# Optimization experiments

Measured on AMD Instinct MI355X. Metric: run time of the kernel, lower is better.

## Reference

```python
import jax, jax.numpy as jnp
import numpy as np
import math

NHEADS = 8


def pos_encoding_2d(d_model, H, W):
    dm = d_model // 2
    div = jnp.exp(jnp.arange(0, dm, 2, dtype=jnp.float32) * (-math.log(10000.0) / dm))  # [dm//2]
    pw = jnp.arange(W, dtype=jnp.float32)[:, None] * div  # [W, dm//2]
    ph = jnp.arange(H, dtype=jnp.float32)[:, None] * div  # [H, dm//2]
    pe = jnp.zeros((d_model, H, W), jnp.float32)
    pe = pe.at[0:dm:2].set(jnp.broadcast_to(jnp.sin(pw).T[:, None, :], (dm // 2, H, W)))
    pe = pe.at[1:dm:2].set(jnp.broadcast_to(jnp.cos(pw).T[:, None, :], (dm // 2, H, W)))
    pe = pe.at[dm::2].set(jnp.broadcast_to(jnp.sin(ph).T[:, :, None], (dm // 2, H, W)))
    pe = pe.at[dm + 1::2].set(jnp.broadcast_to(jnp.cos(ph).T[:, :, None], (dm // 2, H, W)))
    return pe


def conv_same(x, w, b):
    y = jax.lax.conv_general_dilated(x, w, (1, 1), 'SAME',
                                     dimension_numbers=('NCHW', 'OIHW', 'NCHW'))
    return y + b[None, :, None, None]


def layernorm(x, g, b, eps=1e-5):
    mu = x.mean(-1, keepdims=True)
    var = ((x - mu) ** 2).mean(-1, keepdims=True)
    return (x - mu) / jnp.sqrt(var + eps) * g + b


def setup_inputs() -> dict:
    key = jax.random.key(0)
    B, C, H, W = 8, 256, 32, 32
    KQV, NH, K = 64, NHEADS, 3
    ks = jax.random.split(key, 16)
    s_conv = 1.0 / math.sqrt(C * K * K)
    s_lin = 1.0 / math.sqrt(NH * KQV)
    s_ff = 1.0 / math.sqrt(C)
    return {
        'x': jax.random.normal(ks[0], (B, C, H, W), jnp.float32),
        'Wk': jax.random.normal(ks[1], (NH * KQV, C, K, K), jnp.float32) * s_conv,
        'bk': jax.random.normal(ks[2], (NH * KQV,), jnp.float32) * s_conv,
        'Wq': jax.random.normal(ks[3], (NH * KQV, C, K, K), jnp.float32) * s_conv,
        'bq': jax.random.normal(ks[4], (NH * KQV,), jnp.float32) * s_conv,
        'Wv': jax.random.normal(ks[5], (NH * KQV, C, K, K), jnp.float32) * s_conv,
        'bv': jax.random.normal(ks[6], (NH * KQV,), jnp.float32) * s_conv,
        'Wproj': jax.random.normal(ks[7], (C, NH * KQV), jnp.float32) * s_lin,
        'bproj': jax.random.normal(ks[8], (C,), jnp.float32) * s_lin,
        'ln_g': jnp.ones((C,), jnp.float32),
        'ln_b': jnp.zeros((C,), jnp.float32),
        'W1': jax.random.normal(ks[9], (C, C), jnp.float32) * s_ff,
        'b1': jax.random.normal(ks[10], (C,), jnp.float32) * s_ff,
        'W2': jax.random.normal(ks[11], (C, C), jnp.float32) * s_ff,
        'b2': jax.random.normal(ks[12], (C,), jnp.float32) * s_ff,
    }


def reference(x, Wk, bk, Wq, bq, Wv, bv, Wproj, bproj, ln_g, ln_b, W1, b1, W2, b2):
    B, C, H, W = x.shape
    N = H * W
    pe = pos_encoding_2d(C, H, W)
    xp = x + pe[None]                                   # [B,C,H,W]
    xflat = xp.reshape(B, C, N).transpose(0, 2, 1)      # [B,N,C]

    def heads(w, b):
        return conv_same(xp, w, b).reshape(B, NHEADS, -1, N)  # [B,h,c,N]

    k = heads(Wk, bk)
    q = heads(Wq, bq)
    v = heads(Wv, bv)
    scores = jnp.einsum('bhcn,bhcm->bhnm', k, q) / N    # K^T Q / N, [B,h,N,N]
    sm = jax.nn.softmax(scores, axis=1)                 # Softmax2d -> over HEAD dim (faithful)
    att = jnp.einsum('bhnm,bhcm->bhnc', sm, v)          # [B,h,N,c]
    att = att.transpose(0, 2, 3, 1).reshape(B, N, -1)   # [B,N,c*h] (channel-major, head-minor)
    attproj = att @ Wproj.T + bproj                     # [B,N,C]
    addnormed = layernorm(xflat + attproj, ln_g, ln_b)
    h1 = addnormed @ W1.T + b1
    h1 = jnp.where(h1 > 0, h1, 0.1 * h1)                # LeakyReLU(0.1)
    h2 = h1 @ W2.T + b2
    out = layernorm(h2 + addnormed, ln_g, ln_b)         # same LN params reused (faithful)
    return out.transpose(0, 2, 1).reshape(B, C, H, W)
```

## Files before the change

kernel.cpp:

```cpp
#include <hip/hip_runtime.h>
#include <stdint.h>

typedef __attribute__((ext_vector_type(8))) short short8;
typedef __attribute__((ext_vector_type(4))) short s16x4;
typedef __attribute__((ext_vector_type(4))) float f32x4;

#define DEVI __device__ __forceinline__

#if __has_builtin(__builtin_amdgcn_mfma_f32_16x16x16_bf16)
#define MFMA16(a, b, c) __builtin_amdgcn_mfma_f32_16x16x16_bf16(a, b, c, 0, 0, 0)
#else
#define MFMA16(a, b, c) __builtin_amdgcn_mfma_f32_16x16x16bf16_1k(a, b, c, 0, 0, 0)
#endif

DEVI unsigned short f2bf(float f) {
  union { float f; uint32_t u; } v; v.f = f;
  return (unsigned short)((v.u + 0x7fffu + ((v.u >> 16) & 1u)) >> 16);
}

DEVI float bf2f(uint32_t hi16) {
  union { uint32_t u; float f; } v; v.u = hi16;
  return v.f;
}

DEVI uint32_t pkbf(float a, float b) {
  union { float f; uint32_t u; } x, y; x.f = a; y.f = b;
  return ((x.u + 0x8000u) >> 16) | (((y.u + 0x8000u) >> 16) << 16);
}

DEVI void gload_lds16(const void* g, void* l) {
  __builtin_amdgcn_global_load_lds(
      (const __attribute__((address_space(1))) uint32_t*)g,
      (__attribute__((address_space(3))) uint32_t*)l, 16, 0, 0);
}

__global__ void k_petab(float* __restrict__ T, float* __restrict__ zp) {
  int c = threadIdx.x;
  zp[c] = 0.0f;
  int idx = ((c >= 128) ? c - 128 : c) >> 1;
  float freq = expf(-(float)idx * (logf(10000.0f) / 64.0f));
  for (int p = 0; p < 32; ++p) {
    float ang = (float)p * freq;
    T[c * 32 + p] = (c & 1) ? cosf(ang) : sinf(ang);
  }
}

__global__ __launch_bounds__(256) void k_xpt(const float* __restrict__ x,
                                             const float* __restrict__ T,
                                             unsigned short* __restrict__ xpt_bf,
                                             float* __restrict__ xpt_f) {
  __shared__ __align__(16) float tile[32][36];
  const int b = blockIdx.z, c0 = blockIdx.x * 32, n0 = blockIdx.y * 32;
  const int t = threadIdx.x;
  {
    const int cl = t >> 3, ng = (t & 7) * 4;
    const int c = c0 + cl;
    float4 v = *(const float4*)(x + ((size_t)b * 256 + c) * 1024 + n0 + ng);
    float p0, p1, p2, p3;
    if (c < 128) {
      p0 = T[c * 32 + ng + 0]; p1 = T[c * 32 + ng + 1];
      p2 = T[c * 32 + ng + 2]; p3 = T[c * 32 + ng + 3];
    } else {
      p0 = p1 = p2 = p3 = T[c * 32 + (n0 >> 5)];
    }
    tile[ng + 0][cl] = v.x + p0;
    tile[ng + 1][cl] = v.y + p1;
    tile[ng + 2][cl] = v.z + p2;
    tile[ng + 3][cl] = v.w + p3;
  }
  __syncthreads();
  {
    const int nl = t >> 3, cg = (t & 7) * 4;
    float o0 = tile[nl][cg + 0], o1 = tile[nl][cg + 1];
    float o2 = tile[nl][cg + 2], o3 = tile[nl][cg + 3];
    size_t row = (size_t)b * 1024 + n0 + nl;
    *(float4*)(xpt_f + row * 256 + c0 + cg) = make_float4(o0, o1, o2, o3);
    uint32_t lo = (uint32_t)f2bf(o0) | ((uint32_t)f2bf(o1) << 16);
    uint32_t hi = (uint32_t)f2bf(o2) | ((uint32_t)f2bf(o3) << 16);
    *(uint2*)(xpt_bf + row * 256 + c0 + cg) = make_uint2(lo, hi);
  }
}

__global__ void k_packall(const float* __restrict__ Wk, const float* __restrict__ Wq,
                          const float* __restrict__ Wv, const float* __restrict__ bk,
                          const float* __restrict__ bq, const float* __restrict__ bv,
                          const float* __restrict__ Wproj, const float* __restrict__ W1,
                          const float* __restrict__ W2, unsigned short* __restrict__ Wpack,
                          float* __restrict__ bias_kqv, unsigned short* __restrict__ WprojP,
                          unsigned short* __restrict__ W1b, unsigned short* __restrict__ W2b) {
  int bid = blockIdx.x;
  if (bid < 13824) {
    int i = bid * 256 + threadIdx.x;
    if (i >= 1536 * 2304) return;
    int o = i / 2304, kn = i % 2304;
    int ci = kn & 255, khw = kn >> 8;
    const float* src = (o < 512) ? Wk : ((o < 1024) ? Wq : Wv);
    int oo = o & 511;
    Wpack[i] = f2bf(src[((size_t)oo * 256 + ci) * 9 + khw]);
  } else {
    int i = (bid - 13824) * 256 + threadIdx.x;
    if (i < 1536)
      bias_kqv[i] = (i < 512) ? bk[i] : ((i < 1024) ? bq[i - 512] : bv[i - 1024]);
    {
      int j = i >> 9, f = i & 511;
      int h = f >> 6, c = f & 63;
      unsigned short v = f2bf(Wproj[(size_t)j * 512 + c * 8 + h]);
      WprojP[(size_t)j * 1024 + f] = v;
      WprojP[(size_t)j * 1024 + 512 + f] = v;
    }
    if (i < 65536) {
      W1b[i] = f2bf(W1[i]);
      W2b[i] = f2bf(W2[i]);
    }
  }
}

__global__ __launch_bounds__(256, 2) void k_gemm_conv(const unsigned short* __restrict__ xpt,
                                                      const unsigned short* __restrict__ Wp,
                                                      unsigned short* __restrict__ kqv,
                                                      const float* __restrict__ bias,
                                                      const char* __restrict__ zp) {
  __shared__ __align__(16) unsigned short As[2][128 * 64];
  __shared__ __align__(16) unsigned short Bs[2][192 * 64];
  const int tid = threadIdx.x, l = tid & 63, w = tid >> 6;
  const int wm = w >> 1, wn = w & 1, g = l >> 4, ln = l & 15;
  const int m0 = blockIdx.x * 128, n0 = blockIdx.y * 192;
  const int swz = (l & 7) ^ (l >> 3);

  const char* pAbase[4];
#pragma unroll
  for (int j = 0; j < 4; ++j) {
    int r = m0 + (w * 4 + j) * 8 + (l >> 3);
    pAbase[j] = (const char*)xpt + ((size_t)r * 256 + swz * 8) * 2;
  }
  const char* pB0 = (const char*)Wp +
                    ((size_t)(n0 + w * 48 + (l >> 3)) * 2304 + swz * 8) * 2;

  f32x4 acc[4][6] = {};
  int vmask = 0;
  int aoff = 0;

  auto setTap = [&](int tap) {
    int d3 = (tap * 11) >> 5;
    int dy = d3 - 1, dx = tap - d3 * 3 - 1;
    aoff = (dy * 32 + dx) * 512;
    int m = 0;
#pragma unroll
    for (int j = 0; j < 4; ++j) {
      int r = m0 + (w * 4 + j) * 8 + (l >> 3);
      int y = ((r >> 5) & 31) + dy;
      int x = (r & 31) + dx;
      if (((unsigned)y < 32u) && ((unsigned)x < 32u)) m |= (1 << j);
    }
    vmask = m;
  };

  auto STAGE = [&](int buf, int kb) {
#pragma unroll
    for (int j = 0; j < 4; ++j) {
      const char* a = (vmask & (1 << j)) ? (pAbase[j] + aoff) : zp;
      gload_lds16(a, (char*)As + buf * 16384 + (w * 4 + j) * 1024);
    }
#pragma unroll
    for (int j = 0; j < 6; ++j) {
      gload_lds16(pB0 + j * 36864 + kb, (char*)Bs + buf * 24576 + (w * 6 + j) * 1024);
    }
  };

  auto COMPUTE = [&](int buf) {
    const char* Ab2 = (const char*)As + buf * 16384;
    const char* Bb2 = (const char*)Bs + buf * 24576;
#pragma unroll
    for (int kk = 0; kk < 2; ++kk) {
      short8 af[4], bfr[6];
#pragma unroll
      for (int fm = 0; fm < 4; ++fm)
        af[fm] = *(const short8*)(Ab2 + (wm * 64 + fm * 16 + ln) * 128 +
                                  (((kk * 4 + g) ^ (ln & 7)) * 16));
#pragma unroll
      for (int fn = 0; fn < 6; ++fn)
        bfr[fn] = *(const short8*)(Bb2 + (wn * 96 + fn * 16 + ln) * 128 +
                                   (((kk * 4 + g) ^ (ln & 7)) * 16));
#pragma unroll
      for (int fm = 0; fm < 4; ++fm)
#pragma unroll
        for (int fn = 0; fn < 6; ++fn)
          acc[fm][fn] = __builtin_amdgcn_mfma_f32_16x16x32_bf16(af[fm], bfr[fn], acc[fm][fn], 0, 0, 0);
    }
  };

  setTap(0);
  STAGE(0, 0);
  aoff += 128;
  int kb = 128;
  for (int s = 0; s < 36; ++s) {
    const int buf = s & 1;
    if (s < 35) {
      if (((s + 1) & 3) == 0) setTap((s + 1) >> 2);
      STAGE(buf ^ 1, kb);
      kb += 128;
      aoff += 128;
      asm volatile("s_waitcnt vmcnt(10)" ::: "memory");
    } else {
      asm volatile("s_waitcnt vmcnt(0)" ::: "memory");
    }
    __builtin_amdgcn_s_barrier();
    __builtin_amdgcn_sched_barrier(0);
    COMPUTE(buf);
    asm volatile("s_waitcnt lgkmcnt(0)" ::: "memory");
    __builtin_amdgcn_s_barrier();
    __builtin_amdgcn_sched_barrier(0);
  }

#pragma unroll
  for (int fm = 0; fm < 4; ++fm)
#pragma unroll
    for (int fn = 0; fn < 6; ++fn) {
      int col = n0 + wn * 96 + fn * 16 + ln;
      float bb = bias[col];
#pragma unroll
      for (int r = 0; r < 4; ++r) {
        int row = m0 + wm * 64 + fm * 16 + g * 4 + r;
        kqv[(size_t)row * 1536 + col] = f2bf(acc[fm][fn][r] + bb);
      }
    }
}

__global__ __launch_bounds__(256) void k_ffn1(const unsigned short* __restrict__ A,
                                              const unsigned short* __restrict__ B,
                                              unsigned short* __restrict__ Cout,
                                              const float* __restrict__ bias) {
  __shared__ __align__(16) unsigned short As[128 * 64];
  __shared__ __align__(16) unsigned short Bs[64 * 64];
  const int tid = threadIdx.x, l = tid & 63, w = tid >> 6;
  const int g = l >> 4, ln = l & 15;
  const int m0 = blockIdx.x * 128, n0 = blockIdx.y * 64;
  const int swz = (l & 7) ^ (l >> 3);
  f32x4 acc[2][4] = {};

  for (int kt = 0; kt < 256; kt += 64) {
#pragma unroll
    for (int j = 0; j < 4; ++j) {
      int seg = w * 4 + j;
      int r8 = seg * 8 + (l >> 3);
      gload_lds16((const char*)A + ((size_t)(m0 + r8) * 256 + kt + swz * 8) * 2,
                  (char*)As + seg * 1024);
    }
#pragma unroll
    for (int j = 0; j < 2; ++j) {
      int seg = w * 2 + j;
      int r8 = seg * 8 + (l >> 3);
      gload_lds16((const char*)B + ((size_t)(n0 + r8) * 256 + kt + swz * 8) * 2,
                  (char*)Bs + seg * 1024);
    }
    __syncthreads();
#pragma unroll
    for (int kk = 0; kk < 2; ++kk) {
      short8 af[2], bfr[4];
#pragma unroll
      for (int fm = 0; fm < 2; ++fm)
        af[fm] = *(const short8*)((const char*)As + (w * 32 + fm * 16 + ln) * 128 +
                                  (((kk * 4 + g) ^ (ln & 7)) * 16));
#pragma unroll
      for (int fn = 0; fn < 4; ++fn)
        bfr[fn] = *(const short8*)((const char*)Bs + (fn * 16 + ln) * 128 +
                                   (((kk * 4 + g) ^ (ln & 7)) * 16));
#pragma unroll
      for (int fm = 0; fm < 2; ++fm)
#pragma unroll
        for (int fn = 0; fn < 4; ++fn)
          acc[fm][fn] = __builtin_amdgcn_mfma_f32_16x16x32_bf16(af[fm], bfr[fn], acc[fm][fn], 0, 0, 0);
    }
    __syncthreads();
  }

#pragma unroll
  for (int fm = 0; fm < 2; ++fm)
#pragma unroll
    for (int fn = 0; fn < 4; ++fn)
#pragma unroll
      for (int r = 0; r < 4; ++r) {
        int row = m0 + w * 32 + fm * 16 + g * 4 + r;
        int col = n0 + fn * 16 + ln;
        float v = acc[fm][fn][r] + bias[col];
        v = (v > 0.f) ? v : 0.1f * v;
        Cout[(size_t)row * 256 + col] = f2bf(v);
      }
}

__global__ __launch_bounds__(512, 4) void k_attn(const unsigned short* __restrict__ kqv,
                                                 unsigned short* __restrict__ part) {
  __shared__ __align__(16) unsigned short Qs[16][512];
  __shared__ __align__(16) unsigned short Vlin[16][512];
  __shared__ __align__(16) unsigned short Vs[32][16][16];
  __shared__ __align__(16) float sums[4][2][64][4];
  const int tid = threadIdx.x, l = tid & 63, w = tid >> 6;
  const int g = l >> 4, ln = l & 15;
  const int nt = w & 1, hg = w >> 1;
  const int id = blockIdx.x;
  const int b = id & 7, ng = (id >> 3) & 31, ch = id >> 8;
  const int n0 = ng * 32 + nt * 16;
  const int m_base = ch * 512;
  const size_t rowBase = (size_t)b * 1024;
  const float SC = 1.0f / 1024.0f;

  short8 ak[2][2];
#pragma unroll
  for (int hl = 0; hl < 2; ++hl)
#pragma unroll
    for (int kk = 0; kk < 2; ++kk)
      ak[hl][kk] = *(const short8*)&kqv[(rowBase + n0 + ln) * 1536 +
                                        (hg * 2 + hl) * 64 + kk * 32 + g * 8];

  f32x4 acc[2][4] = {};

  const int r0 = w * 2, r1 = w * 2 + 1;
  const char* pRow = (const char*)kqv +
                     (size_t)(rowBase + m_base + r0) * 3072 + 1024 + (size_t)l * 16;
  uint4 q0, q1, v0, v1;

  auto LOADREGS = [&]() {
    q0 = *(const uint4*)pRow;
    v0 = *(const uint4*)(pRow + 1024);
    q1 = *(const uint4*)(pRow + 3072);
    v1 = *(const uint4*)(pRow + 4096);
    pRow += 49152;
  };
  char* const dQ0 = (char*)Qs + r0 * 1024 + ((l ^ (r0 & 7)) * 16);
  char* const dV0 = (char*)Vlin + r0 * 1024 + ((l ^ (r0 & 7)) * 16);
  char* const dQ1 = (char*)Qs + r1 * 1024 + ((l ^ (r1 & 7)) * 16);
  char* const dV1 = (char*)Vlin + r1 * 1024 + ((l ^ (r1 & 7)) * 16);
  auto DSW = [&]() {
    *(uint4*)dQ0 = q0;
    *(uint4*)dV0 = v0;
    *(uint4*)dQ1 = q1;
    *(uint4*)dV1 = v1;
  };

  LOADREGS();
  asm volatile("s_waitcnt vmcnt(0)" ::: "memory");
  DSW();
  asm volatile("s_waitcnt lgkmcnt(0)" ::: "memory");
  __builtin_amdgcn_s_barrier();
  __builtin_amdgcn_sched_barrier(0);

  const uint32_t vsBase = (uint32_t)(uintptr_t)&Vs[0][0][0] + l * 8;

  for (int s = 0; s < 32; ++s) {
    if (s < 31) LOADREGS();

    {
      const int tm = l & 15;
#pragma unroll
      for (int i = 0; i < 2; ++i) {
        int tch = (l >> 4) + w * 4 + i * 32;
        short8 tv = *(const short8*)((const char*)Vlin + tm * 1024 +
                                     ((tch ^ (tm & 7)) * 16));
        *(short8*)((char*)Vs + (tch >> 1) * 512 + tm * 32 + (tch & 1) * 16) = tv;
      }
    }

    f32x4 sv[2] = {};
#pragma unroll
    for (int kk = 0; kk < 2; ++kk)
#pragma unroll
      for (int hl = 0; hl < 2; ++hl) {
        int chq = (hg * 2 + hl) * 8 + kk * 4 + g;
        short8 qa = *(const short8*)((const char*)Qs + ln * 1024 +
                                     ((chq ^ (ln & 7)) * 16));
        sv[hl] = __builtin_amdgcn_mfma_f32_16x16x32_bf16(qa, ak[hl][kk], sv[hl], 0, 0, 0);
      }

    f32x4 e0, e1, ps;
#pragma unroll
    for (int j = 0; j < 4; ++j) {
      e0[j] = __expf(sv[0][j] * SC);
      e1[j] = __expf(sv[1][j] * SC);
      ps[j] = e0[j] + e1[j];
    }
    *(f32x4*)&sums[hg][nt][l][0] = ps;
    asm volatile("s_waitcnt lgkmcnt(0)" ::: "memory");
    __builtin_amdgcn_s_barrier();
    __builtin_amdgcn_sched_barrier(0);

    f32x4 tot = ps;
#pragma unroll
    for (int d = 1; d < 4; ++d) {
      f32x4 o = *(const f32x4*)&sums[(hg + d) & 3][nt][l][0];
      tot[0] += o[0]; tot[1] += o[1]; tot[2] += o[2]; tot[3] += o[3];
    }
    f32x4 inv;
#pragma unroll
    for (int j = 0; j < 4; ++j) inv[j] = __builtin_amdgcn_rcpf(tot[j]);

    s16x4 vf[8];
#pragma unroll
    for (int hl = 0; hl < 2; ++hl) {
      uint32_t ah = vsBase + (hg * 2 + hl) * 2048;
      asm volatile("ds_read_b64_tr_b16 %0, %1" : "=v"(vf[hl * 4 + 0]) : "v"(ah));
      asm volatile("ds_read_b64_tr_b16 %0, %1 offset:512" : "=v"(vf[hl * 4 + 1]) : "v"(ah));
      asm volatile("ds_read_b64_tr_b16 %0, %1 offset:1024" : "=v"(vf[hl * 4 + 2]) : "v"(ah));
      asm volatile("ds_read_b64_tr_b16 %0, %1 offset:1536" : "=v"(vf[hl * 4 + 3]) : "v"(ah));
    }
    asm volatile("s_waitcnt lgkmcnt(0)" ::: "memory");
    __builtin_amdgcn_sched_barrier(0);
    union { uint32_t u[2]; s16x4 v4; } pc0, pc1;
    pc0.u[0] = pkbf(e0[0] * inv[0], e0[1] * inv[1]);
    pc0.u[1] = pkbf(e0[2] * inv[2], e0[3] * inv[3]);
    pc1.u[0] = pkbf(e1[0] * inv[0], e1[1] * inv[1]);
    pc1.u[1] = pkbf(e1[2] * inv[2], e1[3] * inv[3]);
#pragma unroll
    for (int cf = 0; cf < 4; ++cf) {
      acc[0][cf] = MFMA16(vf[cf], pc0.v4, acc[0][cf]);
      acc[1][cf] = MFMA16(vf[4 + cf], pc1.v4, acc[1][cf]);
    }

    if (s < 31) {
      asm volatile("s_waitcnt vmcnt(0)" ::: "memory");
      DSW();
    }
    asm volatile("s_waitcnt lgkmcnt(0)" ::: "memory");
    __builtin_amdgcn_s_barrier();
    __builtin_amdgcn_sched_barrier(0);
  }

  const size_t outBase = (size_t)ch * 8192 * 512 + (rowBase + n0 + ln) * 512;
#pragma unroll
  for (int hl = 0; hl < 2; ++hl)
#pragma unroll
    for (int cf = 0; cf < 4; ++cf)
#pragma unroll
      for (int r2 = 0; r2 < 2; ++r2) {
        int c = (hg * 2 + hl) * 64 + cf * 16 + g * 4 + r2 * 2;
        uint32_t u = (uint32_t)f2bf(acc[hl][cf][2 * r2]) |
                     ((uint32_t)f2bf(acc[hl][cf][2 * r2 + 1]) << 16);
        *(uint32_t*)&part[outBase + c] = u;
      }
}

__global__ __launch_bounds__(256) void k_projln(const unsigned short* __restrict__ part,
                                                const unsigned short* __restrict__ Wp,
                                                const float* __restrict__ bias,
                                                const float* __restrict__ resid,
                                                const float* __restrict__ lg,
                                                const float* __restrict__ lb,
                                                float* __restrict__ out_f,
                                                unsigned short* __restrict__ out_b) {
  __shared__ __align__(16) unsigned short As[32 * 64];
  __shared__ __align__(16) unsigned short Bs[256 * 64];
  __shared__ float rsum[4][32][2];
  const int tid = threadIdx.x, l = tid & 63, w = tid >> 6;
  const int g4 = l >> 4, ln = l & 15;
  const int m0 = blockIdx.x * 32;
  const int swz = (l & 7) ^ (l >> 3);
  f32x4 acc[2][4] = {};

  for (int kt = 0; kt < 1024; kt += 64) {
    gload_lds16((const char*)part + (((size_t)(kt >> 9) * 8192 * 512) +
                                     (size_t)(m0 + w * 8 + (l >> 3)) * 512 +
                                     (kt & 511) + swz * 8) * 2,
                (char*)As + w * 1024);
#pragma unroll
    for (int j = 0; j < 8; ++j) {
      int seg = w * 8 + j;
      gload_lds16((const char*)Wp + ((size_t)(seg * 8 + (l >> 3)) * 1024 + kt + swz * 8) * 2,
                  (char*)Bs + seg * 1024);
    }
    __syncthreads();
#pragma unroll
    for (int kk = 0; kk < 2; ++kk) {
      short8 af[2], bfr[4];
#pragma unroll
      for (int fm = 0; fm < 2; ++fm)
        af[fm] = *(const short8*)((const char*)As + (fm * 16 + ln) * 128 +
                                  (((kk * 4 + g4) ^ (ln & 7)) * 16));
#pragma unroll
      for (int fn = 0; fn < 4; ++fn)
        bfr[fn] = *(const short8*)((const char*)Bs + (w * 64 + fn * 16 + ln) * 128 +
                                   (((kk * 4 + g4) ^ (ln & 7)) * 16));
#pragma unroll
      for (int fm = 0; fm < 2; ++fm)
#pragma unroll
        for (int fn = 0; fn < 4; ++fn)
          acc[fm][fn] = __builtin_amdgcn_mfma_f32_16x16x32_bf16(af[fm], bfr[fn], acc[fm][fn], 0, 0, 0);
    }
    __syncthreads();
  }

  float vals[2][4][4];
#pragma unroll
  for (int fm = 0; fm < 2; ++fm)
#pragma unroll
    for (int r = 0; r < 4; ++r) {
      int row_l = fm * 16 + g4 * 4 + r;
      float s = 0.f, q = 0.f;
#pragma unroll
      for (int fn = 0; fn < 4; ++fn) {
        int col = w * 64 + fn * 16 + ln;
        float v = acc[fm][fn][r] + bias[col] + resid[(size_t)(m0 + row_l) * 256 + col];
        vals[fm][fn][r] = v;
        s += v;
        q += v * v;
      }
#pragma unroll
      for (int o = 1; o < 16; o <<= 1) {
        s += __shfl_xor(s, o, 64);
        q += __shfl_xor(q, o, 64);
      }
      if (ln == 0) {
        rsum[w][row_l][0] = s;
        rsum[w][row_l][1] = q;
      }
    }
  __syncthreads();

#pragma unroll
  for (int fm = 0; fm < 2; ++fm)
#pragma unroll
    for (int r = 0; r < 4; ++r) {
      int row_l = fm * 16 + g4 * 4 + r;
      float s = rsum[0][row_l][0] + rsum[1][row_l][0] + rsum[2][row_l][0] + rsum[3][row_l][0];
      float q = rsum[0][row_l][1] + rsum[1][row_l][1] + rsum[2][row_l][1] + rsum[3][row_l][1];
      float mu = s * (1.0f / 256.0f);
      float rstd = rsqrtf(q * (1.0f / 256.0f) - mu * mu + 1e-5f);
      size_t rowOff = (size_t)(m0 + row_l) * 256;
#pragma unroll
      for (int fn = 0; fn < 4; ++fn) {
        int col = w * 64 + fn * 16 + ln;
        float o = (vals[fm][fn][r] - mu) * rstd * lg[col] + lb[col];
        out_f[rowOff + col] = o;
        out_b[rowOff + col] = f2bf(o);
      }
    }
}

__global__ __launch_bounds__(256) void k_ffn2out(const unsigned short* __restrict__ h1,
                                                 const unsigned short* __restrict__ W2b,
                                                 const float* __restrict__ b2,
                                                 const float* __restrict__ addnf,
                                                 const float* __restrict__ lg,
                                                 const float* __restrict__ lb,
                                                 float* __restrict__ out) {
  __shared__ __align__(16) unsigned short As[32 * 64];
  __shared__ __align__(16) unsigned short Bs[256 * 64];
  __shared__ __align__(16) float Tt[256][33];
  __shared__ float rsum[4][32][2];
  const int tid = threadIdx.x, l = tid & 63, w = tid >> 6;
  const int g4 = l >> 4, ln = l & 15;
  const int m0 = blockIdx.x * 32;
  const int swz = (l & 7) ^ (l >> 3);
  f32x4 acc[2][4] = {};

  for (int kt = 0; kt < 256; kt += 64) {
    gload_lds16((const char*)h1 + ((size_t)(m0 + w * 8 + (l >> 3)) * 256 + kt + swz * 8) * 2,
                (char*)As + w * 1024);
#pragma unroll
    for (int j = 0; j < 8; ++j) {
      int seg = w * 8 + j;
      gload_lds16((const char*)W2b + ((size_t)(seg * 8 + (l >> 3)) * 256 + kt + swz * 8) * 2,
                  (char*)Bs + seg * 1024);
    }
    __syncthreads();
#pragma unroll
    for (int kk = 0; kk < 2; ++kk) {
      short8 af[2], bfr[4];
#pragma unroll
      for (int fm = 0; fm < 2; ++fm)
        af[fm] = *(const short8*)((const char*)As + (fm * 16 + ln) * 128 +
                                  (((kk * 4 + g4) ^ (ln & 7)) * 16));
#pragma unroll
      for (int fn = 0; fn < 4; ++fn)
        bfr[fn] = *(const short8*)((const char*)Bs + (w * 64 + fn * 16 + ln) * 128 +
                                   (((kk * 4 + g4) ^ (ln & 7)) * 16));
#pragma unroll
      for (int fm = 0; fm < 2; ++fm)
#pragma unroll
        for (int fn = 0; fn < 4; ++fn)
          acc[fm][fn] = __builtin_amdgcn_mfma_f32_16x16x32_bf16(af[fm], bfr[fn], acc[fm][fn], 0, 0, 0);
    }
    __syncthreads();
  }

  float vals[2][4][4];
#pragma unroll
  for (int fm = 0; fm < 2; ++fm)
#pragma unroll
    for (int r = 0; r < 4; ++r) {
      int row_l = fm * 16 + g4 * 4 + r;
      float s = 0.f, q = 0.f;
#pragma unroll
      for (int fn = 0; fn < 4; ++fn) {
        int col = w * 64 + fn * 16 + ln;
        float v = acc[fm][fn][r] + b2[col] + addnf[(size_t)(m0 + row_l) * 256 + col];
        vals[fm][fn][r] = v;
        s += v;
        q += v * v;
      }
#pragma unroll
      for (int o = 1; o < 16; o <<= 1) {
        s += __shfl_xor(s, o, 64);
        q += __shfl_xor(q, o, 64);
      }
      if (ln == 0) {
        rsum[w][row_l][0] = s;
        rsum[w][row_l][1] = q;
      }
    }
  __syncthreads();

#pragma unroll
  for (int fm = 0; fm < 2; ++fm)
#pragma unroll
    for (int r = 0; r < 4; ++r) {
      int row_l = fm * 16 + g4 * 4 + r;
      float s = rsum[0][row_l][0] + rsum[1][row_l][0] + rsum[2][row_l][0] + rsum[3][row_l][0];
      float q = rsum[0][row_l][1] + rsum[1][row_l][1] + rsum[2][row_l][1] + rsum[3][row_l][1];
      float mu = s * (1.0f / 256.0f);
      float rstd = rsqrtf(q * (1.0f / 256.0f) - mu * mu + 1e-5f);
#pragma unroll
      for (int fn = 0; fn < 4; ++fn) {
        int col = w * 64 + fn * 16 + ln;
        Tt[col][row_l] = (vals[fm][fn][r] - mu) * rstd * lg[col] + lb[col];
      }
    }
  __syncthreads();

  const int bimg = m0 >> 10, nn0 = m0 & 1023;
#pragma unroll
  for (int i = 0; i < 8; ++i) {
    int c = i * 32 + (tid >> 3);
    int ng = (tid & 7) * 4;
    float4 o = make_float4(Tt[c][ng], Tt[c][ng + 1], Tt[c][ng + 2], Tt[c][ng + 3]);
    *(float4*)&out[((size_t)bimg * 256 + c) * 1024 + nn0 + ng] = o;
  }
}

extern "C" void kernel_launch(void* const* d_in, const int* in_sizes, int n_in,
                              void* d_out, int out_size, void* d_ws, size_t ws_size,
                              hipStream_t stream) {
  const float* x     = (const float*)d_in[0];
  const float* Wk    = (const float*)d_in[1];
  const float* bk    = (const float*)d_in[2];
  const float* Wq    = (const float*)d_in[3];
  const float* bq    = (const float*)d_in[4];
  const float* Wv    = (const float*)d_in[5];
  const float* bv    = (const float*)d_in[6];
  const float* Wproj = (const float*)d_in[7];
  const float* bproj = (const float*)d_in[8];
  const float* ln_g  = (const float*)d_in[9];
  const float* ln_b  = (const float*)d_in[10];
  const float* W1    = (const float*)d_in[11];
  const float* b1    = (const float*)d_in[12];
  const float* W2    = (const float*)d_in[13];
  const float* b2    = (const float*)d_in[14];

  char* ws = (char*)d_ws;
  constexpr size_t OFF_XPTB  = 0;
  constexpr size_t OFF_XPTF  = OFF_XPTB  + (size_t)8192 * 256 * 2;
  constexpr size_t OFF_WPACK = OFF_XPTF  + (size_t)8192 * 256 * 4;
  constexpr size_t OFF_BIAS  = OFF_WPACK + (size_t)1536 * 2304 * 2;
  constexpr size_t OFF_WPROJ = OFF_BIAS  + (size_t)1536 * 4;
  constexpr size_t OFF_W1B   = OFF_WPROJ + (size_t)256 * 1024 * 2;
  constexpr size_t OFF_W2B   = OFF_W1B   + (size_t)256 * 256 * 2;
  constexpr size_t OFF_PET   = OFF_W2B   + (size_t)256 * 256 * 2;
  constexpr size_t OFF_ZERO  = OFF_PET   + (size_t)256 * 32 * 4;
  constexpr size_t OFF_KQV   = OFF_ZERO  + 1024;
  constexpr size_t OFF_PART  = OFF_KQV   + (size_t)8192 * 1536 * 2;
  constexpr size_t OFF_ADDNF = OFF_PART  + (size_t)2 * 8192 * 512 * 2;
  constexpr size_t OFF_ADDNB = OFF_ADDNF + (size_t)8192 * 256 * 4;
  constexpr size_t OFF_H1    = OFF_ADDNB + (size_t)8192 * 256 * 2;

  (void)in_sizes; (void)n_in; (void)out_size; (void)ws_size;

  const char* zp = (const char*)(ws + OFF_ZERO);

  k_petab<<<1, 256, 0, stream>>>((float*)(ws + OFF_PET), (float*)(ws + OFF_ZERO));
  k_xpt<<<dim3(8, 32, 8), 256, 0, stream>>>(x, (const float*)(ws + OFF_PET),
                                            (unsigned short*)(ws + OFF_XPTB),
                                            (float*)(ws + OFF_XPTF));
  k_packall<<<14336, 256, 0, stream>>>(Wk, Wq, Wv, bk, bq, bv, Wproj, W1, W2,
                                       (unsigned short*)(ws + OFF_WPACK),
                                       (float*)(ws + OFF_BIAS),
                                       (unsigned short*)(ws + OFF_WPROJ),
                                       (unsigned short*)(ws + OFF_W1B),
                                       (unsigned short*)(ws + OFF_W2B));
  k_gemm_conv<<<dim3(64, 8), 256, 0, stream>>>(
      (const unsigned short*)(ws + OFF_XPTB), (const unsigned short*)(ws + OFF_WPACK),
      (unsigned short*)(ws + OFF_KQV), (const float*)(ws + OFF_BIAS), zp);
  k_attn<<<dim3(512), 512, 0, stream>>>((const unsigned short*)(ws + OFF_KQV),
                                        (unsigned short*)(ws + OFF_PART));
  k_projln<<<256, 256, 0, stream>>>((const unsigned short*)(ws + OFF_PART),
                                    (const unsigned short*)(ws + OFF_WPROJ), bproj,
                                    (const float*)(ws + OFF_XPTF), ln_g, ln_b,
                                    (float*)(ws + OFF_ADDNF), (unsigned short*)(ws + OFF_ADDNB));
  k_ffn1<<<dim3(64, 4), 256, 0, stream>>>(
      (const unsigned short*)(ws + OFF_ADDNB), (const unsigned short*)(ws + OFF_W1B),
      (unsigned short*)(ws + OFF_H1), b1);
  k_ffn2out<<<256, 256, 0, stream>>>((const unsigned short*)(ws + OFF_H1),
                                     (const unsigned short*)(ws + OFF_W2B), b2,
                                     (const float*)(ws + OFF_ADDNF), ln_g, ln_b,
                                     (float*)d_out);
}
```

Baseline: 187.6 us.

## Write V directly in transposed padded layout, double-buffer it, and swizzle conv block order

In the attention kernel, V rows are now stored straight from registers into a padded, double-buffered shared-memory layout suited to the transposed ds_read, removing the per-iteration Vlin-to-Vs shuffle pass. The row stride is padded to avoid bank conflicts. MFMA sections are wrapped in s_setprio to favour matrix issue across waves. The conv GEMM remaps block IDs so that neighbouring blocks share weight tiles, which should improve L2 reuse. This adds some LDS footprint for the double buffer and changes the write-side bank pattern.

```diff
diff --git a/kernel.cpp b/kernel.cpp
--- a/kernel.cpp
+++ b/kernel.cpp
@@ -124,7 +124,9 @@
   __shared__ __align__(16) unsigned short Bs[2][192 * 64];
   const int tid = threadIdx.x, l = tid & 63, w = tid >> 6;
   const int wm = w >> 1, wn = w & 1, g = l >> 4, ln = l & 15;
-  const int m0 = blockIdx.x * 128, n0 = blockIdx.y * 192;
+  const int id = blockIdx.x + (blockIdx.y << 6);
+  const int nid = ((id & 7) << 6) + (id >> 3);
+  const int m0 = (nid & 63) * 128, n0 = (nid >> 6) * 192;
   const int swz = (l & 7) ^ (l >> 3);
 
   const char* pAbase[4];
@@ -291,8 +293,7 @@
 __global__ __launch_bounds__(512, 4) void k_attn(const unsigned short* __restrict__ kqv,
                                                  unsigned short* __restrict__ part) {
   __shared__ __align__(16) unsigned short Qs[16][512];
-  __shared__ __align__(16) unsigned short Vlin[16][512];
-  __shared__ __align__(16) unsigned short Vs[32][16][16];
+  __shared__ __align__(16) char VsRaw[2][32 * 544];
   __shared__ __align__(16) float sums[4][2][64][4];
   const int tid = threadIdx.x, l = tid & 63, w = tid >> 6;
   const int g = l >> 4, ln = l & 15;
@@ -327,40 +328,29 @@
     pRow += 49152;
   };
   char* const dQ0 = (char*)Qs + r0 * 1024 + ((l ^ (r0 & 7)) * 16);
-  char* const dV0 = (char*)Vlin + r0 * 1024 + ((l ^ (r0 & 7)) * 16);
   char* const dQ1 = (char*)Qs + r1 * 1024 + ((l ^ (r1 & 7)) * 16);
-  char* const dV1 = (char*)Vlin + r1 * 1024 + ((l ^ (r1 & 7)) * 16);
-  auto DSW = [&]() {
+  const uint32_t vOff = (uint32_t)(l >> 1) * 544 + (uint32_t)(l & 1) * 16;
+  auto DSW = [&](int vbuf) {
     *(uint4*)dQ0 = q0;
-    *(uint4*)dV0 = v0;
     *(uint4*)dQ1 = q1;
-    *(uint4*)dV1 = v1;
+    char* vb = VsRaw[vbuf];
+    *(uint4*)(vb + vOff + r0 * 32) = v0;
+    *(uint4*)(vb + vOff + r1 * 32) = v1;
   };
 
   LOADREGS();
   asm volatile("s_waitcnt vmcnt(0)" ::: "memory");
-  DSW();
+  DSW(0);
   asm volatile("s_waitcnt lgkmcnt(0)" ::: "memory");
   __builtin_amdgcn_s_barrier();
   __builtin_amdgcn_sched_barrier(0);
 
-  const uint32_t vsBase = (uint32_t)(uintptr_t)&Vs[0][0][0] + l * 8;
-
   for (int s = 0; s < 32; ++s) {
+    const int buf = s & 1;
     if (s < 31) LOADREGS();
 
-    {
-      const int tm = l & 15;
-#pragma unroll
-      for (int i = 0; i < 2; ++i) {
-        int tch = (l >> 4) + w * 4 + i * 32;
-        short8 tv = *(const short8*)((const char*)Vlin + tm * 1024 +
-                                     ((tch ^ (tm & 7)) * 16));
-        *(short8*)((char*)Vs + (tch >> 1) * 512 + tm * 32 + (tch & 1) * 16) = tv;
-      }
-    }
-
     f32x4 sv[2] = {};
+    __builtin_amdgcn_s_setprio(1);
 #pragma unroll
     for (int kk = 0; kk < 2; ++kk)
 #pragma unroll
@@ -370,6 +360,7 @@
                                      ((chq ^ (ln & 7)) * 16));
         sv[hl] = __builtin_amdgcn_mfma_f32_16x16x32_bf16(qa, ak[hl][kk], sv[hl], 0, 0, 0);
       }
+    __builtin_amdgcn_s_setprio(0);
 
     f32x4 e0, e1, ps;
 #pragma unroll
@@ -393,14 +384,15 @@
 #pragma unroll
     for (int j = 0; j < 4; ++j) inv[j] = __builtin_amdgcn_rcpf(tot[j]);
 
+    const uint32_t vsB = (uint32_t)(uintptr_t)VsRaw[buf] + l * 8;
     s16x4 vf[8];
 #pragma unroll
     for (int hl = 0; hl < 2; ++hl) {
-      uint32_t ah = vsBase + (hg * 2 + hl) * 2048;
+      uint32_t ah = vsB + (hg * 2 + hl) * 2176;
       asm volatile("ds_read_b64_tr_b16 %0, %1" : "=v"(vf[hl * 4 + 0]) : "v"(ah));
-      asm volatile("ds_read_b64_tr_b16 %0, %1 offset:512" : "=v"(vf[hl * 4 + 1]) : "v"(ah));
-      asm volatile("ds_read_b64_tr_b16 %0, %1 offset:1024" : "=v"(vf[hl * 4 + 2]) : "v"(ah));
-      asm volatile("ds_read_b64_tr_b16 %0, %1 offset:1536" : "=v"(vf[hl * 4 + 3]) : "v"(ah));
+      asm volatile("ds_read_b64_tr_b16 %0, %1 offset:544" : "=v"(vf[hl * 4 + 1]) : "v"(ah));
+      asm volatile("ds_read_b64_tr_b16 %0, %1 offset:1088" : "=v"(vf[hl * 4 + 2]) : "v"(ah));
+      asm volatile("ds_read_b64_tr_b16 %0, %1 offset:1632" : "=v"(vf[hl * 4 + 3]) : "v"(ah));
     }
     asm volatile("s_waitcnt lgkmcnt(0)" ::: "memory");
     __builtin_amdgcn_sched_barrier(0);
@@ -409,15 +401,17 @@
     pc0.u[1] = pkbf(e0[2] * inv[2], e0[3] * inv[3]);
     pc1.u[0] = pkbf(e1[0] * inv[0], e1[1] * inv[1]);
     pc1.u[1] = pkbf(e1[2] * inv[2], e1[3] * inv[3]);
+    __builtin_amdgcn_s_setprio(1);
 #pragma unroll
     for (int cf = 0; cf < 4; ++cf) {
       acc[0][cf] = MFMA16(vf[cf], pc0.v4, acc[0][cf]);
       acc[1][cf] = MFMA16(vf[4 + cf], pc1.v4, acc[1][cf]);
     }
+    __builtin_amdgcn_s_setprio(0);
 
     if (s < 31) {
       asm volatile("s_waitcnt vmcnt(0)" ::: "memory");
-      DSW();
+      DSW(buf ^ 1);
     }
     asm volatile("s_waitcnt lgkmcnt(0)" ::: "memory");
     __builtin_amdgcn_s_barrier();
```

New measurement: 185.7 us. About the same (-1.0%).
